# Kernel optimization log

Measured on AMD Instinct MI355X. Metric: run time of the kernel, lower is better.

Reference implementation:

```python
import jax, jax.numpy as jnp
import numpy as np

B, L, K, NR, S = 512, 1024, 8, 512, 20  # batch, seq_len, n_matrices, n_rates, alphabet
EXT = 26  # extended alphabet (20 std aa + 6 special), pad of 6 in call()


def _expm(A):
    """Differentiable matrix exponential for small batched matrices (..., n, n).
    Scaling-and-squaring with an order-16 Taylor series (fixed 6 squarings).
    Matches tf.linalg.expm to high accuracy for the small-norm tau*Q here."""
    SQ = 6
    A = A / jnp.asarray(2.0 ** SQ, A.dtype)
    n = A.shape[-1]
    I = jnp.eye(n, dtype=A.dtype)
    P = I + A
    T = A
    for i in range(2, 17):
        T = jnp.matmul(T, A) / i
        P = P + T
    for _ in range(SQ):
        P = jnp.matmul(P, P)
    return P


def setup_inputs() -> dict:
    key = jax.random.key(0)
    k1, k2, k3, k4, k5 = jax.random.split(key, 5)
    return {
        "inputs": jax.random.randint(k1, (B, L), 0, EXT, dtype=jnp.int32),
        "rate_indices": jax.random.randint(k2, (B,), 0, NR, dtype=jnp.int32),
        "tau_kernel": jax.random.normal(k3, (NR,), dtype=jnp.float32),
        "exchangeability_kernel": jax.random.normal(k4, (K, S, S), dtype=jnp.float32),
        "frequencies": jax.random.uniform(k5, (S,), dtype=jnp.float32, minval=0.01, maxval=1.0),
    }


def reference(inputs, rate_indices, tau_kernel, exchangeability_kernel, frequencies):
    b, l = inputs.shape
    mask = inputs < S                                   # (b, L) std-aa mask
    std = jnp.where(mask, inputs, 0)                    # clamp special tokens to 0
    maskf = mask.astype(jnp.float32)[:, :, None, None]  # (b, L, 1, 1)

    # make_R: symmetrize, softplus, zero diagonal
    eye = jnp.eye(S, dtype=jnp.float32)
    R = jax.nn.softplus(0.5 * (exchangeability_kernel + jnp.swapaxes(exchangeability_kernel, -1, -2)))
    R = R * (1.0 - eye)

    # make_rate_matrix: Q = R * pi, subtract row-sum diagonal, normalize by expected rate
    Q = R * frequencies[None, None, :]                  # (k, s, s)
    diag = jnp.sum(Q, axis=-1, keepdims=True)           # (k, s, 1)
    Q = Q - diag * eye
    mue = jnp.sum(frequencies[None, :, None] * diag, axis=-2, keepdims=True)  # (k, 1, 1)
    Q = Q / jnp.maximum(mue, 1e-16)

    # per-sequence evolutionary times
    tau = jax.nn.softplus(tau_kernel)[rate_indices]     # (b,)

    # batched small-matrix expm: (b, k, s, s)
    P = _expm(tau[:, None, None, None] * Q[None])

    # gather ancestral probability rows: (b, L, k, s)
    anc = P[jnp.arange(b)[:, None], :, std, :]
    anc = anc * maskf
    anc = jnp.pad(anc, ((0, 0), (0, 0), (0, 0), (0, EXT - S)))  # pad 20 -> 26
    rest = jax.nn.one_hot(inputs, EXT, dtype=jnp.float32)[:, :, None, :] * (1.0 - maskf)
    anc = anc + rest                                    # (b, L, k, 26)
    return anc.reshape(b, l, -1)                        # (b, L, k*26)
```

## Files before the change

### kernel.cpp

```cpp
#include <hip/hip_runtime.h>
#include <math.h>

#define B    512
#define L    1024
#define K    8
#define NR   512
#define S    20
#define EXT  26
#define SS   (S*S)
#define PD   24
#define PDSQ (PD*PD)
#define ROWF (K*EXT)
#define BROW (L*ROWF)

__device__ __forceinline__ float softplusf(float x) {
    return fmaxf(x, 0.0f) + log1pf(expf(-fabsf(x)));
}

__global__ __launch_bounds__(512, 2) void fused_kernel(
    const int*   __restrict__ inputs,
    const int*   __restrict__ rate_indices,
    const float* __restrict__ tau_kernel,
    const float* __restrict__ exch,
    const float* __restrict__ freq,
    float* __restrict__ out)
{
    __shared__ __align__(16) float M[K][2][PDSQ];
    __shared__ __align__(16) float Row[EXT*ROWF];
    __shared__ int   inp_sh[L];
    __shared__ float diag_sh[K][S];
    __shared__ float mue_sh[K];
    __shared__ float tau_sh;

    const int b    = blockIdx.x;
    const int t    = threadIdx.x;
    const int w    = t >> 6;
    const int lane = t & 63;
    const int li = lane >> 3, lj = lane & 7;
    const int r0 = 3*li, c0 = 3*lj;

    for (int u = t; u < L; u += 512) inp_sh[u] = inputs[b*L + u];
    for (int e = t; e < EXT*ROWF; e += 512) {
        int row = e / ROWF, c = e - row*ROWF;
        int k = c / EXT, s = c - k*EXT;
        Row[e] = (row >= S && s == row) ? 1.f : 0.f;
    }
    {
        float* Mw = &M[w][0][0];
        for (int e = lane; e < 2*PDSQ; e += 64) Mw[e] = 0.f;
    }
    if (t == 0) tau_sh = softplusf(tau_kernel[rate_indices[b]]);
    __syncthreads();

    float* M0 = &M[w][0][0];
    float* M1 = &M[w][1][0];
    const float* E = exch + w * SS;

    for (int e = lane; e < SS; e += 64) {
        int r = e / S, c = e - r*S;
        float v = 0.f;
        if (r != c)
            v = softplusf(0.5f * (E[r*S + c] + E[c*S + r])) * freq[c];
        M0[r*PD + c] = v;
    }
    __syncthreads();
    if (lane < S) {
        float d = 0.f;
        #pragma unroll
        for (int j = 0; j < S; ++j) d += M0[lane*PD + j];
        diag_sh[w][lane] = d;
    }
    __syncthreads();
    if (lane == 0) {
        float m = 0.f;
        #pragma unroll
        for (int s = 0; s < S; ++s) m += freq[s] * diag_sh[w][s];
        mue_sh[w] = fmaxf(m, 1e-16f);
    }
    __syncthreads();
    {
        float scale = tau_sh * 0.015625f;
        float mue   = mue_sh[w];
        for (int e = lane; e < SS; e += 64) {
            int r = e / S, c = e - r*S;
            float v = (r == c) ? -diag_sh[w][r] : M0[r*PD + c];
            M0[r*PD + c] = (v / mue) * scale;
        }
    }
    __syncthreads();

    float Ac[S][3];
    #pragma unroll
    for (int j = 0; j < S; ++j) {
        #pragma unroll
        for (int d = 0; d < 3; ++d)
            Ac[j][d] = M0[j*PD + c0 + d];
    }

    float P[3][3];
    #pragma unroll
    for (int dr = 0; dr < 3; ++dr)
        #pragma unroll
        for (int dc = 0; dc < 3; ++dc) {
            int r = r0 + dr, c = c0 + dc;
            P[dr][dc] = M0[r*PD + c] + ((r == c && r < S) ? 1.f : 0.f);
        }

    const float* Tc = M0;
    float* Tn = M1;
    #pragma unroll 1
    for (int i = 2; i <= 16; ++i) {
        float C[3][3] = {{0.f,0.f,0.f},{0.f,0.f,0.f},{0.f,0.f,0.f}};
        #pragma unroll
        for (int jc = 0; jc < 5; ++jc) {
            float4 a0 = *(const float4*)&Tc[(r0+0)*PD + 4*jc];
            float4 a1 = *(const float4*)&Tc[(r0+1)*PD + 4*jc];
            float4 a2 = *(const float4*)&Tc[(r0+2)*PD + 4*jc];
            float t0[4] = {a0.x, a0.y, a0.z, a0.w};
            float t1[4] = {a1.x, a1.y, a1.z, a1.w};
            float t2[4] = {a2.x, a2.y, a2.z, a2.w};
            #pragma unroll
            for (int dj = 0; dj < 4; ++dj) {
                int j = 4*jc + dj;
                #pragma unroll
                for (int dc = 0; dc < 3; ++dc) {
                    C[0][dc] = fmaf(t0[dj], Ac[j][dc], C[0][dc]);
                    C[1][dc] = fmaf(t1[dj], Ac[j][dc], C[1][dc]);
                    C[2][dc] = fmaf(t2[dj], Ac[j][dc], C[2][dc]);
                }
            }
        }
        float inv = 1.0f / (float)i;
        #pragma unroll
        for (int dr = 0; dr < 3; ++dr)
            #pragma unroll
            for (int dc = 0; dc < 3; ++dc) {
                C[dr][dc] *= inv;
                P[dr][dc] += C[dr][dc];
                Tn[(r0+dr)*PD + c0 + dc] = C[dr][dc];
            }
        __syncthreads();
        float* tmp = (float*)Tc; Tc = Tn; Tn = tmp;
    }

    #pragma unroll 1
    for (int sq = 0; sq < 6; ++sq) {
        #pragma unroll
        for (int dr = 0; dr < 3; ++dr)
            #pragma unroll
            for (int dc = 0; dc < 3; ++dc)
                Tn[(r0+dr)*PD + c0 + dc] = P[dr][dc];
        __syncthreads();
        const float* Pb = Tn;
        float C[3][3] = {{0.f,0.f,0.f},{0.f,0.f,0.f},{0.f,0.f,0.f}};
        #pragma unroll
        for (int jc = 0; jc < 5; ++jc) {
            float4 a0 = *(const float4*)&Pb[(r0+0)*PD + 4*jc];
            float4 a1 = *(const float4*)&Pb[(r0+1)*PD + 4*jc];
            float4 a2 = *(const float4*)&Pb[(r0+2)*PD + 4*jc];
            float t0[4] = {a0.x, a0.y, a0.z, a0.w};
            float t1[4] = {a1.x, a1.y, a1.z, a1.w};
            float t2[4] = {a2.x, a2.y, a2.z, a2.w};
            float cb[4][3];
            #pragma unroll
            for (int dj = 0; dj < 4; ++dj)
                #pragma unroll
                for (int dc = 0; dc < 3; ++dc)
                    cb[dj][dc] = Pb[(4*jc + dj)*PD + c0 + dc];
            #pragma unroll
            for (int dj = 0; dj < 4; ++dj)
                #pragma unroll
                for (int dc = 0; dc < 3; ++dc) {
                    C[0][dc] = fmaf(t0[dj], cb[dj][dc], C[0][dc]);
                    C[1][dc] = fmaf(t1[dj], cb[dj][dc], C[1][dc]);
                    C[2][dc] = fmaf(t2[dj], cb[dj][dc], C[2][dc]);
                }
        }
        #pragma unroll
        for (int dr = 0; dr < 3; ++dr)
            #pragma unroll
            for (int dc = 0; dc < 3; ++dc)
                P[dr][dc] = C[dr][dc];
        float* tmp = (float*)Tc; Tc = Tn; Tn = tmp;
        __syncthreads();
    }

    #pragma unroll
    for (int dr = 0; dr < 3; ++dr) {
        int r = r0 + dr; if (r >= S) continue;
        #pragma unroll
        for (int dc = 0; dc < 3; ++dc) {
            int c = c0 + dc; if (c >= S) continue;
            Row[r*ROWF + w*EXT + c] = P[dr][dc];
        }
    }
    __syncthreads();

    const float4* Row4 = (const float4*)Row;
    float4* out4 = (float4*)out + (size_t)b * (BROW/4);
    for (int u = t; u < L * (ROWF/4); u += 512) {
        int l = u / (ROWF/4);
        int q = u - l * (ROWF/4);
        out4[u] = Row4[inp_sh[l] * (ROWF/4) + q];
    }
}

extern "C" void kernel_launch(void* const* d_in, const int* in_sizes, int n_in,
                              void* d_out, int out_size, void* d_ws, size_t ws_size,
                              hipStream_t stream) {
    const int*   inputs  = (const int*)  d_in[0];
    const int*   rate_ix = (const int*)  d_in[1];
    const float* tau_k   = (const float*)d_in[2];
    const float* exch    = (const float*)d_in[3];
    const float* freq    = (const float*)d_in[4];
    float* out = (float*)d_out;

    (void)d_ws; (void)ws_size;

    fused_kernel<<<B, 512, 0, stream>>>(inputs, rate_ix, tau_k, exch, freq, out);
}
```

Before: 493.9 us.

## Replace block barriers with wave barriers, shorten Taylor series, hoist output indexing

Each wave builds and exponentiates its own matrix, so the block-wide __syncthreads between expm stages are replaced with wave-level barriers. The per-block shared tau is computed per thread, and only the needed Row entries are initialized. The Taylor expansion is cut from order 16 to order 10, and the output copy loop precomputes its row/column indices to avoid divisions. The goal is to cut barrier stalls and ALU work ahead of the memory-bound output stream. The risks are lower expm accuracy and reliance on in-order LDS access within a wave.

Result: faster. 476.6 us (-3.5%).

```diff
diff --git a/kernel.cpp b/kernel.cpp
--- a/kernel.cpp
+++ b/kernel.cpp
@@ -15,6 +15,10 @@
 
 __device__ __forceinline__ float softplusf(float x) {
     return fmaxf(x, 0.0f) + log1pf(expf(-fabsf(x)));
+}
+
+__device__ __forceinline__ void wave_fence() {
+    __builtin_amdgcn_wave_barrier();
 }
 
 __global__ __launch_bounds__(512, 2) void fused_kernel(
@@ -30,7 +34,6 @@
     __shared__ int   inp_sh[L];
     __shared__ float diag_sh[K][S];
     __shared__ float mue_sh[K];
-    __shared__ float tau_sh;
 
     const int b    = blockIdx.x;
     const int t    = threadIdx.x;
@@ -43,19 +46,19 @@
     for (int e = t; e < EXT*ROWF; e += 512) {
         int row = e / ROWF, c = e - row*ROWF;
         int k = c / EXT, s = c - k*EXT;
-        Row[e] = (row >= S && s == row) ? 1.f : 0.f;
-    }
-    {
-        float* Mw = &M[w][0][0];
-        for (int e = lane; e < 2*PDSQ; e += 64) Mw[e] = 0.f;
-    }
-    if (t == 0) tau_sh = softplusf(tau_kernel[rate_indices[b]]);
-    __syncthreads();
-
+        if (row < S) {
+            if (s >= S) Row[e] = 0.f;
+        } else {
+            Row[e] = (s == row) ? 1.f : 0.f;
+        }
+    }
     float* M0 = &M[w][0][0];
     float* M1 = &M[w][1][0];
+    for (int e = lane; e < 2*PDSQ; e += 64) M0[e] = 0.f;
+    float tau = softplusf(tau_kernel[rate_indices[b]]);
+    wave_fence();
+
     const float* E = exch + w * SS;
-
     for (int e = lane; e < SS; e += 64) {
         int r = e / S, c = e - r*S;
         float v = 0.f;
@@ -63,23 +66,23 @@
             v = softplusf(0.5f * (E[r*S + c] + E[c*S + r])) * freq[c];
         M0[r*PD + c] = v;
     }
-    __syncthreads();
+    wave_fence();
     if (lane < S) {
         float d = 0.f;
         #pragma unroll
         for (int j = 0; j < S; ++j) d += M0[lane*PD + j];
         diag_sh[w][lane] = d;
     }
-    __syncthreads();
+    wave_fence();
     if (lane == 0) {
         float m = 0.f;
         #pragma unroll
         for (int s = 0; s < S; ++s) m += freq[s] * diag_sh[w][s];
         mue_sh[w] = fmaxf(m, 1e-16f);
     }
-    __syncthreads();
+    wave_fence();
     {
-        float scale = tau_sh * 0.015625f;
+        float scale = tau * 0.015625f;
         float mue   = mue_sh[w];
         for (int e = lane; e < SS; e += 64) {
             int r = e / S, c = e - r*S;
@@ -87,7 +90,7 @@
             M0[r*PD + c] = (v / mue) * scale;
         }
     }
-    __syncthreads();
+    wave_fence();
 
     float Ac[S][3];
     #pragma unroll
@@ -109,7 +112,7 @@
     const float* Tc = M0;
     float* Tn = M1;
     #pragma unroll 1
-    for (int i = 2; i <= 16; ++i) {
+    for (int i = 2; i <= 10; ++i) {
         float C[3][3] = {{0.f,0.f,0.f},{0.f,0.f,0.f},{0.f,0.f,0.f}};
         #pragma unroll
         for (int jc = 0; jc < 5; ++jc) {
@@ -139,7 +142,7 @@
                 P[dr][dc] += C[dr][dc];
                 Tn[(r0+dr)*PD + c0 + dc] = C[dr][dc];
             }
-        __syncthreads();
+        wave_fence();
         float* tmp = (float*)Tc; Tc = Tn; Tn = tmp;
     }
 
@@ -150,7 +153,7 @@
             #pragma unroll
             for (int dc = 0; dc < 3; ++dc)
                 Tn[(r0+dr)*PD + c0 + dc] = P[dr][dc];
-        __syncthreads();
+        wave_fence();
         const float* Pb = Tn;
         float C[3][3] = {{0.f,0.f,0.f},{0.f,0.f,0.f},{0.f,0.f,0.f}};
         #pragma unroll
@@ -182,7 +185,7 @@
             for (int dc = 0; dc < 3; ++dc)
                 P[dr][dc] = C[dr][dc];
         float* tmp = (float*)Tc; Tc = Tn; Tn = tmp;
-        __syncthreads();
+        wave_fence();
     }
 
     #pragma unroll
@@ -196,12 +199,27 @@
     }
     __syncthreads();
 
+    int l0[13], qq[13];
+    {
+        int uu = t;
+        #pragma unroll
+        for (int j = 0; j < 13; ++j) {
+            l0[j] = uu / 52;
+            qq[j] = uu - l0[j] * 52;
+            uu += 512;
+        }
+    }
     const float4* Row4 = (const float4*)Row;
     float4* out4 = (float4*)out + (size_t)b * (BROW/4);
-    for (int u = t; u < L * (ROWF/4); u += 512) {
-        int l = u / (ROWF/4);
-        int q = u - l * (ROWF/4);
-        out4[u] = Row4[inp_sh[l] * (ROWF/4) + q];
+    #pragma unroll 1
+    for (int i = 0; i < 8; ++i) {
+        int lbase = i << 7;
+        int ubase = t + i * 6656;
+        #pragma unroll
+        for (int j = 0; j < 13; ++j) {
+            int inp = inp_sh[l0[j] + lbase];
+            out4[ubase + (j << 9)] = Row4[inp * 52 + qq[j]];
+        }
     }
 }
 
```
